# Performance work log

Hardware: AMD Instinct MI355X
Metric: run time of the kernel (lower is better)

The kernel has to match this reference:

```python
import jax, jax.numpy as jnp
import numpy as np

H = 16
D = 64
WIN = 512
THETA = 10000.0


def _rope(x):
    # x: [B, H, T, D]
    T = x.shape[2]
    inv = 1.0 / (THETA ** (jnp.arange(0, D, 2, dtype=jnp.float32) / D))  # [D/2]
    f = jnp.arange(T, dtype=jnp.float32)[:, None] * inv[None, :]          # [T, D/2]
    f = jnp.concatenate([f, f], axis=-1)                                  # [T, D]
    cos, sin = jnp.cos(f), jnp.sin(f)
    x1, x2 = jnp.split(x, 2, axis=-1)
    rot = jnp.concatenate([-x2, x1], axis=-1)
    return x * cos + rot * sin


def setup_inputs() -> dict:
    key = jax.random.key(0)
    ks = jax.random.split(key, 9)
    C = H * D
    s = 0.02
    return {
        "x":  jax.random.normal(ks[0], (2, 2048, C), dtype=jnp.float32),
        "Wq": jax.random.normal(ks[1], (C, C), dtype=jnp.float32) * s,
        "bq": jnp.zeros((C,), dtype=jnp.float32),
        "Wk": jax.random.normal(ks[2], (C, C), dtype=jnp.float32) * s,
        "bk": jnp.zeros((C,), dtype=jnp.float32),
        "Wv": jax.random.normal(ks[3], (C, C), dtype=jnp.float32) * s,
        "bv": jnp.zeros((C,), dtype=jnp.float32),
        "Wo": jax.random.normal(ks[4], (C, C), dtype=jnp.float32) * s,
        "bo": jnp.zeros((C,), dtype=jnp.float32),
    }


def reference(x, Wq, bq, Wk, bk, Wv, bv, Wo, bo):
    B, T, C = x.shape
    def split_heads(y):
        return y.reshape(B, T, H, D).transpose(0, 2, 1, 3)  # [B,H,T,D]
    q = split_heads(x @ Wq + bq)
    k = split_heads(x @ Wk + bk)
    v = split_heads(x @ Wv + bv)
    q = _rope(q)
    k = _rope(k)
    scores = jnp.einsum('bhqd,bhkd->bhqk', q, k) * (1.0 / np.sqrt(D))
    # the original module does NOT apply a causal mask, only the window).
    idx = jnp.arange(T)
    allowed = idx[None, :] >= idx[:, None] - (WIN - 1)      # [T, T] bool
    scores = jnp.where(allowed[None, None], scores, -jnp.inf)
    attn = jax.nn.softmax(scores, axis=-1)
    out = jnp.einsum('bhqk,bhkd->bhqd', attn, v)
    out = out.transpose(0, 2, 1, 3).reshape(B, T, C)
    return out @ Wo + bo
```

## Files before the change

kernel.cpp:

```cpp
#include <hip/hip_runtime.h>
#include <hip/hip_bf16.h>
#include <math.h>

#define Bsz 2
#define Tt  2048
#define Cc  1024
#define Hh  16
#define Dd  64

typedef __attribute__((ext_vector_type(8))) short short8v;
typedef __attribute__((ext_vector_type(4))) short short4v;
typedef __attribute__((ext_vector_type(8))) _Float16 half8v;
typedef __attribute__((ext_vector_type(4))) float f32x4;
typedef __attribute__((ext_vector_type(16))) float f32x16;
typedef __attribute__((ext_vector_type(4))) unsigned int uint4v;

static __device__ __forceinline__ short f2h(float f) {
  _Float16 h = (_Float16)f;
  return __builtin_bit_cast(short, h);
}
static __device__ __forceinline__ float h2f(short s) {
  _Float16 h = __builtin_bit_cast(_Float16, s);
  return (float)h;
}
static __device__ __forceinline__ void gll16(const void* g, void* l) {
  __builtin_amdgcn_global_load_lds((const __attribute__((address_space(1))) unsigned int*)g,
                                   (__attribute__((address_space(3))) unsigned int*)l, 16, 0, 0);
}

__global__ __launch_bounds__(256) void prep(const float* __restrict__ x,
                                            const float* __restrict__ Wq,
                                            const float* __restrict__ Wk,
                                            const float* __restrict__ Wv,
                                            const float* __restrict__ Wo,
                                            short* __restrict__ xh,
                                            short* __restrict__ WTh,
                                            float* __restrict__ rt) {
  __shared__ float T[64][68];
  const int bid = blockIdx.x;
  const int tid = threadIdx.x;

  if (bid < 2048) {
    int t = bid * 256 + tid;
    const float* s = x + (size_t)t * 8;
    float4 a = *(const float4*)s, b = *(const float4*)(s + 4);
    short8v h;
    h[0] = f2h(a.x); h[1] = f2h(a.y); h[2] = f2h(a.z); h[3] = f2h(a.w);
    h[4] = f2h(b.x); h[5] = f2h(b.y); h[6] = f2h(b.z); h[7] = f2h(b.w);
    *(short8v*)(xh + (size_t)t * 8) = h;
  } else if (bid < 3072) {
    const int z = (bid - 2048) >> 8;
    const int slot = (bid - 2048) & 255;
    const float* W = z == 0 ? Wq : z == 1 ? Wk : z == 2 ? Wv : Wo;
    short* oh = WTh + (size_t)z * 1048576;
    const int n0 = (slot & 15) * 64, k0 = (slot >> 4) * 64;
#pragma unroll
    for (int i = 0; i < 4; ++i) {
      int s2 = tid + i * 256;
      int r = s2 >> 4, c4 = (s2 & 15) << 2;
      *(float4*)&T[r][c4] = *(const float4*)(W + (size_t)(k0 + r) * Cc + n0 + c4);
    }
    __syncthreads();
#pragma unroll
    for (int i = 0; i < 2; ++i) {
      int s2 = tid + i * 256;
      int nl = s2 >> 3, ks = (s2 & 7) << 3;
      short8v h;
#pragma unroll
      for (int e = 0; e < 8; ++e) h[e] = f2h(T[ks + e][nl]);
      *(short8v*)(oh + (size_t)(n0 + nl) * Cc + k0 + ks) = h;
    }
  } else {
    int idx = (bid - 3072) * 256 + tid;
    int t = idx >> 5, p = idx & 31;
    float inv = exp2f(-(float)p * (13.2877123795494f / 32.f));
    float sn, cs;
    sincosf((float)t * inv, &sn, &cs);
    float2 v; v.x = cs; v.y = sn;
    *(float2*)(rt + (size_t)idx * 2) = v;
  }
}

__device__ __forceinline__ void core128h(const short* __restrict__ Ah,
                                         const short* __restrict__ Bh,
                                         short* AhL, short* BhL,
                                         int row0, int col0, int wv, int lane, f32x4 acc[4][4]) {
  const int l15 = lane & 15, g = lane >> 4;
  const int wr = wv >> 1, wc = wv & 1;

  const int r8 = lane >> 3;
  const int sch = ((lane & 7) ^ r8) << 3;
  size_t aoff[4], boff[4];
#pragma unroll
  for (int gi = 0; gi < 4; ++gi) {
    aoff[gi] = (size_t)(row0 + wv * 32 + 8 * gi + r8) * Cc + sch;
    boff[gi] = (size_t)(col0 + wv * 32 + 8 * gi + r8) * Cc + sch;
  }
  short* dA = AhL + wv * 2048;
  short* dB = BhL + wv * 2048;

  int aL[4][2], bL[4][2];
#pragma unroll
  for (int m = 0; m < 4; ++m)
#pragma unroll
    for (int s = 0; s < 2; ++s) {
      aL[m][s] = (wr * 64 + m * 16 + l15) * 64 + (((4 * s + g) ^ (l15 & 7)) << 3);
      bL[m][s] = (wc * 64 + m * 16 + l15) * 64 + (((4 * s + g) ^ (l15 & 7)) << 3);
    }

  for (int k0 = 0; k0 < Cc; k0 += 64) {
    __syncthreads();
#pragma unroll
    for (int gi = 0; gi < 4; ++gi) {
      gll16(Ah + aoff[gi] + k0, dA + gi * 512);
      gll16(Bh + boff[gi] + k0, dB + gi * 512);
    }
    __syncthreads();
#pragma unroll
    for (int s = 0; s < 2; ++s) {
      half8v a[4], b[4];
#pragma unroll
      for (int m = 0; m < 4; ++m) a[m] = __builtin_bit_cast(half8v, *(short8v*)&AhL[aL[m][s]]);
#pragma unroll
      for (int n = 0; n < 4; ++n) b[n] = __builtin_bit_cast(half8v, *(short8v*)&BhL[bL[n][s]]);
#pragma unroll
      for (int m = 0; m < 4; ++m)
#pragma unroll
        for (int n = 0; n < 4; ++n)
          acc[m][n] = __builtin_amdgcn_mfma_f32_16x16x32_f16(a[m], b[n], acc[m][n], 0, 0, 0);
    }
  }
}

__global__ __launch_bounds__(256, 3) void gemm_qkv(const short* __restrict__ xh,
                                                   const short* __restrict__ WTh,
                                                   const float* __restrict__ bq,
                                                   const float* __restrict__ bk,
                                                   const float* __restrict__ bv,
                                                   const float* __restrict__ rt,
                                                   short* __restrict__ qb,
                                                   short* __restrict__ kb,
                                                   short* __restrict__ vb) {
  __shared__ short AhL[8192], BhL[8192];
  const int mode = blockIdx.y;
  const short* Bh = WTh + (size_t)mode * 1048576;
  const float* bias = mode == 0 ? bq : mode == 1 ? bk : bv;
  short* Y = mode == 0 ? qb : mode == 1 ? kb : vb;

  const int bid = blockIdx.x;
  const int nid = ((bid & 7) << 5) | (bid >> 3);
  const int row0 = (nid >> 3) * 128, col0 = (nid & 7) * 128;
  const int lane = threadIdx.x & 63, wv = threadIdx.x >> 6;
  const int l15 = lane & 15, g = lane >> 4;
  const int wr = wv >> 1, wc = wv & 1;

  f32x4 acc[4][4];
#pragma unroll
  for (int m = 0; m < 4; ++m)
#pragma unroll
    for (int n = 0; n < 4; ++n) acc[m][n] = (f32x4){0.f, 0.f, 0.f, 0.f};

  core128h(xh, Bh, AhL, BhL, row0, col0, wv, lane, acc);

  const int cbase = col0 + wc * 64;
  const int h = cbase >> 6;
  if (mode < 2) {
    const float scale = (mode == 0) ? 0.18033688f : 1.0f;
    const float2* rt2 = (const float2*)rt;
#pragma unroll
    for (int n = 0; n < 2; ++n) {
      const int d = n * 16 + l15;
      const float b0 = bias[cbase + d], b1 = bias[cbase + d + 32];
#pragma unroll
      for (int m = 0; m < 4; ++m)
#pragma unroll
        for (int rr = 0; rr < 4; ++rr) {
          int R = row0 + wr * 64 + m * 16 + g * 4 + rr;
          int bI = R >> 11, t = R & (Tt - 1);
          float2 cssn = rt2[t * 32 + d];
          float v0 = acc[m][n][rr] + b0, v1 = acc[m][n + 2][rr] + b1;
          size_t base = (((size_t)(bI * Hh + h) * Tt + t) << 6) + d;
          Y[base]      = f2h((v0 * cssn.x - v1 * cssn.y) * scale);
          Y[base + 32] = f2h((v1 * cssn.x + v0 * cssn.y) * scale);
        }
    }
  } else {
#pragma unroll
    for (int n = 0; n < 2; ++n) {
      const int d = n * 16 + l15;
      const float b0 = bias[cbase + d], b1 = bias[cbase + d + 32];
#pragma unroll
      for (int m = 0; m < 4; ++m) {
        int R = row0 + wr * 64 + m * 16 + g * 4;
        int bI = R >> 11, t = R & (Tt - 1);
        short4v s0, s1;
#pragma unroll
        for (int rr = 0; rr < 4; ++rr) {
          s0[rr] = f2h(acc[m][n][rr] + b0);
          s1[rr] = f2h(acc[m][n + 2][rr] + b1);
        }
        size_t base = ((size_t)(bI * Hh + h) * Dd);
        *(short4v*)(Y + (base + d) * Tt + t)      = s0;
        *(short4v*)(Y + (base + d + 32) * Tt + t) = s1;
      }
    }
  }
}

__global__ __launch_bounds__(256, 3) void gemm_out(const short* __restrict__ ah,
                                                   const short* __restrict__ WTo,
                                                   const float* __restrict__ bias,
                                                   float* __restrict__ Y) {
  __shared__ short AhL[8192], BhL[8192];
  const int bid = blockIdx.x;
  const int nid = ((bid & 7) << 5) | (bid >> 3);
  const int row0 = (nid >> 3) * 128, col0 = (nid & 7) * 128;
  const int lane = threadIdx.x & 63, wv = threadIdx.x >> 6;
  const int l15 = lane & 15, g = lane >> 4;
  const int wr = wv >> 1, wc = wv & 1;

  f32x4 acc[4][4];
#pragma unroll
  for (int m = 0; m < 4; ++m)
#pragma unroll
    for (int n = 0; n < 4; ++n) acc[m][n] = (f32x4){0.f, 0.f, 0.f, 0.f};

  core128h(ah, WTo, AhL, BhL, row0, col0, wv, lane, acc);

  const int cbase = col0 + wc * 64;
#pragma unroll
  for (int n = 0; n < 2; ++n) {
    const int ccol = cbase + n * 16 + l15;
    const float b0 = bias[ccol], b1 = bias[ccol + 32];
#pragma unroll
    for (int m = 0; m < 4; ++m)
#pragma unroll
      for (int rr = 0; rr < 4; ++rr) {
        int R = row0 + wr * 64 + m * 16 + g * 4 + rr;
        Y[(size_t)R * Cc + ccol]      = acc[m][n][rr] + b0;
        Y[(size_t)R * Cc + ccol + 32] = acc[m][n + 2][rr] + b1;
      }
  }
}

static __device__ const int JQ2[32] = {0,0, 1,1, 2,2, 3,3, 4,4, 5,5, 6,6, 7,7,
                                       8,8, 9,9, 10,10, 11,11, 12,12, 13,13,
                                       14,14, 15,15};
static __device__ const int JK2[32] = {0,1, 0,1, 0,1, 0,1, 0,1, 0,1, 0,1, 0,1,
                                       0,1, 0,1, 0,1, 0,1, 0,1, 0,1, 0,1, 0,1};

__global__ __launch_bounds__(256, 4) void attn_mfma(const short* __restrict__ q,
                                                    const short* __restrict__ k,
                                                    const short* __restrict__ vT,
                                                    short* __restrict__ ah,
                                                    float* __restrict__ yb,
                                                    float* __restrict__ side) {
  const int n = blockIdx.x;
  const int xcd = n & 7;
  const int t7 = n >> 3;
  const int bhj = t7 & 3;
  const int j = t7 >> 2;
  const int bh = xcd * 4 + bhj;
  const int Q = JQ2[j];
  const int kh = JK2[j];
  const int q0 = Q * 128;

  const int tid = threadIdx.x;
  const int lane = tid & 63;
  const int wv = tid >> 6;
  const int l31 = lane & 31;
  const int hb = lane >> 5;
  const int qbase = q0 + wv * 32;
  const int tq = qbase + l31;

  const short* qgb = q + (size_t)bh * Tt * Dd;
  const short* kgb = k + (size_t)bh * Tt * Dd;
  const short* vgb = vT + (size_t)bh * Dd * Tt;

  const short* qp = qgb + (size_t)tq * Dd + 8 * hb;
  half8v qf[4];
#pragma unroll
  for (int i = 0; i < 4; ++i) qf[i] = __builtin_bit_cast(half8v, *(const short8v*)(qp + 16 * i));

  __shared__ short Klds[2][4096];
  __shared__ short Vt[2][4096];

  const int r8 = lane >> 3;
  const size_t ksrc0 = (size_t)(wv * 16 + r8) * Dd + (((lane & 7) ^ r8) << 3);
  const size_t ksrc1 = ksrc0 + (size_t)8 * Dd;
  const int vlog = ((lane & 7) - r8) & 7;
  const size_t vsrc0 = (size_t)(wv * 16 + r8) * Tt + (vlog << 3);
  const size_t vsrc1 = vsrc0 + (size_t)8 * Tt;

#define STAGE64(BUF, JT)                                                     \
  {                                                                          \
    gll16(kgb + (size_t)(JT) * Dd + ksrc0, &Klds[BUF][wv * 1024]);           \
    gll16(kgb + (size_t)(JT) * Dd + ksrc1, &Klds[BUF][wv * 1024 + 512]);     \
    gll16(vgb + vsrc0 + (JT), &Vt[BUF][wv * 1024]);                          \
    gll16(vgb + vsrc1 + (JT), &Vt[BUF][wv * 1024 + 512]);                    \
  }

  int koff[4], voff[4];
#pragma unroll
  for (int i = 0; i < 4; ++i) {
    koff[i] = l31 * 64 + (((2 * i + hb) ^ (l31 & 7)) << 3);
    voff[i] = l31 * 64 + ((((2 * i + hb) + (l31 & 7)) & 7) << 3);
  }

  f32x16 oacc[2];
#pragma unroll
  for (int t = 0; t < 2; ++t)
#pragma unroll
    for (int r = 0; r < 16; ++r) oacc[t][r] = 0.f;
  float lrun = 0.f;

  const int cs0 = (q0 >= 512) ? (q0 - 511) : 0;
  const int cstart = cs0 & ~63;
  const int nch_b = (Tt - cstart) >> 6;
  const int lower = (nch_b + 1) >> 1;
  const int mystart = cstart + (kh ? (lower << 6) : 0);
  const int myn = kh ? (nch_b - lower) : lower;

  STAGE64(0, mystart);
  __syncthreads();

  int cur = 0;
  for (int ci = 0; ci < myn; ++ci) {
    const int jt = mystart + (ci << 6);

    if (ci + 1 < myn) STAGE64(cur ^ 1, jt + 64);

    const short* kbuf = &Klds[cur][0];
    f32x16 seA, seB;
#pragma unroll
    for (int r = 0; r < 16; ++r) { seA[r] = 0.f; seB[r] = 0.f; }
    __builtin_amdgcn_s_setprio(1);
#pragma unroll
    for (int i = 0; i < 4; ++i) {
      half8v kfA = __builtin_bit_cast(half8v, *(short8v*)&kbuf[koff[i]]);
      seA = __builtin_amdgcn_mfma_f32_32x32x16_f16(kfA, qf[i], seA, 0, 0, 0);
    }
#pragma unroll
    for (int i = 0; i < 4; ++i) {
      half8v kfB = __builtin_bit_cast(half8v, *(short8v*)&kbuf[koff[i] + 2048]);
      seB = __builtin_amdgcn_mfma_f32_32x32x16_f16(kfB, qf[i], seB, 0, 0, 0);
    }
    __builtin_amdgcn_s_setprio(0);

    if (jt < qbase - 480) {
      int th = tq - 511 - jt;
#pragma unroll
      for (int r = 0; r < 16; ++r) {
        int row = (r & 3) + 8 * (r >> 2) + 4 * hb;
        if (row < th) seA[r] = -1e30f;
        if (32 + row < th) seB[r] = -1e30f;
      }
    }

    float pA[16], pB[16];
#pragma unroll
    for (int r = 0; r < 16; ++r) {
      asm("v_exp_f32 %0, %1" : "=v"(pA[r]) : "v"(seA[r]));
      asm("v_exp_f32 %0, %1" : "=v"(pB[r]) : "v"(seB[r]));
    }
    float t0 = 0.f, t1 = 0.f, t2 = 0.f, t3 = 0.f;
#pragma unroll
    for (int r = 0; r < 16; r += 4) {
      t0 += pA[r];     t1 += pA[r + 1]; t2 += pA[r + 2]; t3 += pA[r + 3];
      t0 += pB[r];     t1 += pB[r + 1]; t2 += pB[r + 2]; t3 += pB[r + 3];
    }
    float psum = (t0 + t1) + (t2 + t3);
    psum += __shfl_xor(psum, 32);
    lrun += psum;

    unsigned pa[8], pb[8];
#pragma unroll
    for (int i = 0; i < 8; ++i) {
      pa[i] = __builtin_bit_cast(unsigned, __builtin_amdgcn_cvt_pkrtz(pA[2 * i], pA[2 * i + 1]));
      pb[i] = __builtin_bit_cast(unsigned, __builtin_amdgcn_cvt_pkrtz(pB[2 * i], pB[2 * i + 1]));
    }
    asm volatile("v_permlane32_swap_b32 %0, %1" : "+v"(pa[0]), "+v"(pa[2]));
    asm volatile("v_permlane32_swap_b32 %0, %1" : "+v"(pa[1]), "+v"(pa[3]));
    asm volatile("v_permlane32_swap_b32 %0, %1" : "+v"(pa[4]), "+v"(pa[6]));
    asm volatile("v_permlane32_swap_b32 %0, %1" : "+v"(pa[5]), "+v"(pa[7]));
    asm volatile("v_permlane32_swap_b32 %0, %1" : "+v"(pb[0]), "+v"(pb[2]));
    asm volatile("v_permlane32_swap_b32 %0, %1" : "+v"(pb[1]), "+v"(pb[3]));
    asm volatile("v_permlane32_swap_b32 %0, %1" : "+v"(pb[4]), "+v"(pb[6]));
    asm volatile("v_permlane32_swap_b32 %0, %1" : "+v"(pb[5]), "+v"(pb[7]));
    uint4v fA0, fA1, fB0, fB1;
    fA0[0] = pa[0]; fA0[1] = pa[1]; fA0[2] = pa[2]; fA0[3] = pa[3];
    fA1[0] = pa[4]; fA1[1] = pa[5]; fA1[2] = pa[6]; fA1[3] = pa[7];
    fB0[0] = pb[0]; fB0[1] = pb[1]; fB0[2] = pb[2]; fB0[3] = pb[3];
    fB1[0] = pb[4]; fB1[1] = pb[5]; fB1[2] = pb[6]; fB1[3] = pb[7];
    half8v pfA0 = __builtin_bit_cast(half8v, fA0);
    half8v pfA1 = __builtin_bit_cast(half8v, fA1);
    half8v pfB0 = __builtin_bit_cast(half8v, fB0);
    half8v pfB1 = __builtin_bit_cast(half8v, fB1);

    const short* vbuf = &Vt[cur][0];
    __builtin_amdgcn_s_setprio(1);
#pragma unroll
    for (int t = 0; t < 2; ++t) {
      const int ro = t * 2048;
      half8v v0 = __builtin_bit_cast(half8v, *(short8v*)&vbuf[voff[0] + ro]);
      half8v v1 = __builtin_bit_cast(half8v, *(short8v*)&vbuf[voff[1] + ro]);
      half8v v2 = __builtin_bit_cast(half8v, *(short8v*)&vbuf[voff[2] + ro]);
      half8v v3 = __builtin_bit_cast(half8v, *(short8v*)&vbuf[voff[3] + ro]);
      oacc[t] = __builtin_amdgcn_mfma_f32_32x32x16_f16(v0, pfA0, oacc[t], 0, 0, 0);
      oacc[t] = __builtin_amdgcn_mfma_f32_32x32x16_f16(v1, pfA1, oacc[t], 0, 0, 0);
      oacc[t] = __builtin_amdgcn_mfma_f32_32x32x16_f16(v2, pfB0, oacc[t], 0, 0, 0);
      oacc[t] = __builtin_amdgcn_mfma_f32_32x32x16_f16(v3, pfB1, oacc[t], 0, 0, 0);
    }
    __builtin_amdgcn_s_setprio(0);

    __syncthreads();
    cur ^= 1;
  }

  const float invl = 1.f / lrun;
  const int row = bh * Tt + tq;
  if (hb == 0) side[kh * 65536 + row] = lrun;
  const int bI = bh >> 4, hd = bh & 15;
  if (kh == 0) {
    short* op = ah + ((size_t)(bI * Tt + tq)) * Cc + hd * Dd;
#pragma unroll
    for (int t = 0; t < 2; ++t)
#pragma unroll
      for (int rq = 0; rq < 4; ++rq) {
        short4v hv;
#pragma unroll
        for (int rr = 0; rr < 4; ++rr) hv[rr] = f2h(oacc[t][4 * rq + rr] * invl);
        *(short4v*)(op + 32 * t + 8 * rq + 4 * hb) = hv;
      }
  } else {
    float* yp = yb + (size_t)row * 64;
#pragma unroll
    for (int t = 0; t < 2; ++t)
#pragma unroll
      for (int rq = 0; rq < 4; ++rq) {
        f32x4 o4;
#pragma unroll
        for (int rr = 0; rr < 4; ++rr) o4[rr] = oacc[t][4 * rq + rr] * invl;
        *(f32x4*)(yp + 32 * t + 8 * rq + 4 * hb) = o4;
      }
  }
}

__global__ __launch_bounds__(256) void attn_merge(short* __restrict__ ah,
                                                  const float* __restrict__ yb,
                                                  const float* __restrict__ side) {
  const int bh = blockIdx.y;
  const int idx = blockIdx.x * 256 + threadIdx.x;
  const int tq = idx >> 2;
  const int qd = (idx & 3) << 4;
  const int row = bh * Tt + tq;
  const float l0 = side[row], l1 = side[65536 + row];
  const float inv = 1.f / (l0 + l1);
  const float a0 = l0 * inv, a1 = l1 * inv;

  const int bI = bh >> 4, hd = bh & 15;
  short* op = ah + ((size_t)(bI * Tt + tq)) * Cc + hd * Dd + qd;
  const float* yp = yb + (size_t)row * 64 + qd;

  short8v h0 = *(short8v*)op, h1 = *(short8v*)(op + 8);
  short8v o0, o1;
#pragma unroll
  for (int e = 0; e < 8; ++e) o0[e] = f2h(a0 * h2f(h0[e]) + a1 * yp[e]);
#pragma unroll
  for (int e = 0; e < 8; ++e) o1[e] = f2h(a0 * h2f(h1[e]) + a1 * yp[8 + e]);
  *(short8v*)op = o0;
  *(short8v*)(op + 8) = o1;
}

extern "C" void kernel_launch(void* const* d_in, const int* in_sizes, int n_in,
                              void* d_out, int out_size, void* d_ws, size_t ws_size,
                              hipStream_t stream) {
  const float* x  = (const float*)d_in[0];
  const float* Wq = (const float*)d_in[1];
  const float* bq = (const float*)d_in[2];
  const float* Wk = (const float*)d_in[3];
  const float* bk = (const float*)d_in[4];
  const float* Wv = (const float*)d_in[5];
  const float* bv = (const float*)d_in[6];
  const float* Wo = (const float*)d_in[7];
  const float* bo = (const float*)d_in[8];

  short* ws16 = (short*)d_ws;
  short* xh  = ws16;
  short* WTh = ws16 + 4194304;
  short* qb  = ws16 + 8388608;
  short* kb  = ws16 + 12582912;
  short* vb  = ws16 + 16777216;
  short* ah  = ws16 + 20971520;
  float* yb   = (float*)(ws16 + 25165824);
  float* side = yb + 4194304;
  float* rt   = side + 131072;

  prep<<<3328, 256, 0, stream>>>(x, Wq, Wk, Wv, Wo, xh, WTh, rt);

  gemm_qkv<<<dim3(256, 3), 256, 0, stream>>>(xh, WTh, bq, bk, bv, rt, qb, kb, vb);

  attn_mfma<<<1024, 256, 0, stream>>>(qb, kb, vb, ah, yb, side);
  attn_merge<<<dim3(32, 32), 256, 0, stream>>>(ah, yb, side);

  gemm_out<<<256, 256, 0, stream>>>(ah, WTh + 3 * 1048576, bo, (float*)d_out);
}
```

Before: 114.3 us.

## Split attention KV range three ways, store fp16 partials, retile output GEMM to 128x64

Attention work is split across three key-range chunks per query block instead of two, raising the grid from 1024 to 1536 blocks. Partial outputs for the non-first chunks are stored as fp16 rather than fp32, and the merge kernel combines three partials weighted by their softmax denominators. The output GEMM gets its own inline 128x64 tile loop with 512 blocks and higher occupancy in place of the shared 128x128 core. This aims to fill the GPU better and cut partial-buffer traffic, at the cost of more merge reads, lower precision in the partials and smaller GEMM tiles with less data reuse.

```diff
diff --git a/kernel.cpp b/kernel.cpp
--- a/kernel.cpp
+++ b/kernel.cpp
@@ -207,53 +207,97 @@
   }
 }
 
-__global__ __launch_bounds__(256, 3) void gemm_out(const short* __restrict__ ah,
+__global__ __launch_bounds__(256, 4) void gemm_out(const short* __restrict__ ah,
                                                    const short* __restrict__ WTo,
                                                    const float* __restrict__ bias,
                                                    float* __restrict__ Y) {
-  __shared__ short AhL[8192], BhL[8192];
+  __shared__ short AhL[8192], BhL[4096];
   const int bid = blockIdx.x;
-  const int nid = ((bid & 7) << 5) | (bid >> 3);
-  const int row0 = (nid >> 3) * 128, col0 = (nid & 7) * 128;
+  const int nid = ((bid & 7) << 6) | (bid >> 3);
+  const int row0 = (nid >> 4) * 128, col0 = (nid & 15) * 64;
   const int lane = threadIdx.x & 63, wv = threadIdx.x >> 6;
   const int l15 = lane & 15, g = lane >> 4;
-  const int wr = wv >> 1, wc = wv & 1;
-
-  f32x4 acc[4][4];
-#pragma unroll
-  for (int m = 0; m < 4; ++m)
+
+  const int r8 = lane >> 3;
+  const int sch = ((lane & 7) ^ r8) << 3;
+  size_t aoff[4], boff[2];
+#pragma unroll
+  for (int gi = 0; gi < 4; ++gi)
+    aoff[gi] = (size_t)(row0 + wv * 32 + 8 * gi + r8) * Cc + sch;
+#pragma unroll
+  for (int gi = 0; gi < 2; ++gi)
+    boff[gi] = (size_t)(col0 + wv * 16 + 8 * gi + r8) * Cc + sch;
+  short* dA = AhL + wv * 2048;
+  short* dB = BhL + wv * 1024;
+
+  int aL[2][2], bL[4][2];
+#pragma unroll
+  for (int m = 0; m < 2; ++m)
+#pragma unroll
+    for (int s = 0; s < 2; ++s)
+      aL[m][s] = (wv * 32 + m * 16 + l15) * 64 + (((4 * s + g) ^ (l15 & 7)) << 3);
+#pragma unroll
+  for (int n = 0; n < 4; ++n)
+#pragma unroll
+    for (int s = 0; s < 2; ++s)
+      bL[n][s] = (n * 16 + l15) * 64 + (((4 * s + g) ^ (l15 & 7)) << 3);
+
+  f32x4 acc[2][4];
+#pragma unroll
+  for (int m = 0; m < 2; ++m)
 #pragma unroll
     for (int n = 0; n < 4; ++n) acc[m][n] = (f32x4){0.f, 0.f, 0.f, 0.f};
 
-  core128h(ah, WTo, AhL, BhL, row0, col0, wv, lane, acc);
-
-  const int cbase = col0 + wc * 64;
-#pragma unroll
-  for (int n = 0; n < 2; ++n) {
-    const int ccol = cbase + n * 16 + l15;
-    const float b0 = bias[ccol], b1 = bias[ccol + 32];
-#pragma unroll
-    for (int m = 0; m < 4; ++m)
+  for (int k0 = 0; k0 < Cc; k0 += 64) {
+    __syncthreads();
+#pragma unroll
+    for (int gi = 0; gi < 4; ++gi) gll16(ah + aoff[gi] + k0, dA + gi * 512);
+#pragma unroll
+    for (int gi = 0; gi < 2; ++gi) gll16(WTo + boff[gi] + k0, dB + gi * 512);
+    __syncthreads();
+#pragma unroll
+    for (int s = 0; s < 2; ++s) {
+      half8v a[2], b[4];
+#pragma unroll
+      for (int m = 0; m < 2; ++m) a[m] = __builtin_bit_cast(half8v, *(short8v*)&AhL[aL[m][s]]);
+#pragma unroll
+      for (int n = 0; n < 4; ++n) b[n] = __builtin_bit_cast(half8v, *(short8v*)&BhL[bL[n][s]]);
+#pragma unroll
+      for (int m = 0; m < 2; ++m)
+#pragma unroll
+        for (int n = 0; n < 4; ++n)
+          acc[m][n] = __builtin_amdgcn_mfma_f32_16x16x32_f16(a[m], b[n], acc[m][n], 0, 0, 0);
+    }
+  }
+
+#pragma unroll
+  for (int n = 0; n < 4; ++n) {
+    const int ccol = col0 + n * 16 + l15;
+    const float b0 = bias[ccol];
+#pragma unroll
+    for (int m = 0; m < 2; ++m)
 #pragma unroll
       for (int rr = 0; rr < 4; ++rr) {
-        int R = row0 + wr * 64 + m * 16 + g * 4 + rr;
-        Y[(size_t)R * Cc + ccol]      = acc[m][n][rr] + b0;
-        Y[(size_t)R * Cc + ccol + 32] = acc[m][n + 2][rr] + b1;
+        int R = row0 + wv * 32 + m * 16 + g * 4 + rr;
+        Y[(size_t)R * Cc + ccol] = acc[m][n][rr] + b0;
       }
   }
 }
 
-static __device__ const int JQ2[32] = {0,0, 1,1, 2,2, 3,3, 4,4, 5,5, 6,6, 7,7,
-                                       8,8, 9,9, 10,10, 11,11, 12,12, 13,13,
-                                       14,14, 15,15};
-static __device__ const int JK2[32] = {0,1, 0,1, 0,1, 0,1, 0,1, 0,1, 0,1, 0,1,
-                                       0,1, 0,1, 0,1, 0,1, 0,1, 0,1, 0,1, 0,1};
+static __device__ const int JQ3[48] = {0,0,0, 1,1,1, 2,2,2, 3,3,3, 4,4,4, 5,5,5,
+                                       6,6,6, 7,7,7, 8,8,8, 9,9,9, 10,10,10,
+                                       11,11,11, 12,12,12, 13,13,13, 14,14,14,
+                                       15,15,15};
+static __device__ const int JK3[48] = {0,1,2, 0,1,2, 0,1,2, 0,1,2, 0,1,2, 0,1,2,
+                                       0,1,2, 0,1,2, 0,1,2, 0,1,2, 0,1,2, 0,1,2,
+                                       0,1,2, 0,1,2, 0,1,2, 0,1,2};
 
 __global__ __launch_bounds__(256, 4) void attn_mfma(const short* __restrict__ q,
                                                     const short* __restrict__ k,
                                                     const short* __restrict__ vT,
                                                     short* __restrict__ ah,
-                                                    float* __restrict__ yb,
+                                                    short* __restrict__ p1,
+                                                    short* __restrict__ p2,
                                                     float* __restrict__ side) {
   const int n = blockIdx.x;
   const int xcd = n & 7;
@@ -261,8 +305,8 @@
   const int bhj = t7 & 3;
   const int j = t7 >> 2;
   const int bh = xcd * 4 + bhj;
-  const int Q = JQ2[j];
-  const int kh = JK2[j];
+  const int Q = JQ3[j];
+  const int kh = JK3[j];
   const int q0 = Q * 128;
 
   const int tid = threadIdx.x;
@@ -317,9 +361,10 @@
   const int cs0 = (q0 >= 512) ? (q0 - 511) : 0;
   const int cstart = cs0 & ~63;
   const int nch_b = (Tt - cstart) >> 6;
-  const int lower = (nch_b + 1) >> 1;
-  const int mystart = cstart + (kh ? (lower << 6) : 0);
-  const int myn = kh ? (nch_b - lower) : lower;
+  const int start_i = (nch_b * kh) / 3;
+  const int end_i = (nch_b * (kh + 1)) / 3;
+  const int mystart = cstart + (start_i << 6);
+  const int myn = end_i - start_i;
 
   STAGE64(0, mystart);
   __syncthreads();
@@ -433,41 +478,47 @@
         *(short4v*)(op + 32 * t + 8 * rq + 4 * hb) = hv;
       }
   } else {
-    float* yp = yb + (size_t)row * 64;
+    short* pp = (kh == 1 ? p1 : p2) + (size_t)row * 64;
 #pragma unroll
     for (int t = 0; t < 2; ++t)
 #pragma unroll
       for (int rq = 0; rq < 4; ++rq) {
-        f32x4 o4;
-#pragma unroll
-        for (int rr = 0; rr < 4; ++rr) o4[rr] = oacc[t][4 * rq + rr] * invl;
-        *(f32x4*)(yp + 32 * t + 8 * rq + 4 * hb) = o4;
+        short4v hv;
+#pragma unroll
+        for (int rr = 0; rr < 4; ++rr) hv[rr] = f2h(oacc[t][4 * rq + rr] * invl);
+        *(short4v*)(pp + 32 * t + 8 * rq + 4 * hb) = hv;
       }
   }
 }
 
 __global__ __launch_bounds__(256) void attn_merge(short* __restrict__ ah,
-                                                  const float* __restrict__ yb,
+                                                  const short* __restrict__ p1,
+                                                  const short* __restrict__ p2,
                                                   const float* __restrict__ side) {
   const int bh = blockIdx.y;
   const int idx = blockIdx.x * 256 + threadIdx.x;
   const int tq = idx >> 2;
   const int qd = (idx & 3) << 4;
   const int row = bh * Tt + tq;
-  const float l0 = side[row], l1 = side[65536 + row];
-  const float inv = 1.f / (l0 + l1);
-  const float a0 = l0 * inv, a1 = l1 * inv;
+  const float l0 = side[row], l1 = side[65536 + row], l2 = side[131072 + row];
+  const float inv = 1.f / (l0 + l1 + l2);
+  const float a0 = l0 * inv, a1 = l1 * inv, a2 = l2 * inv;
 
   const int bI = bh >> 4, hd = bh & 15;
   short* op = ah + ((size_t)(bI * Tt + tq)) * Cc + hd * Dd + qd;
-  const float* yp = yb + (size_t)row * 64 + qd;
-
-  short8v h0 = *(short8v*)op, h1 = *(short8v*)(op + 8);
+  const short* r1 = p1 + (size_t)row * 64 + qd;
+  const short* r2 = p2 + (size_t)row * 64 + qd;
+
+  short8v h0 = *(short8v*)op,        h1 = *(short8v*)(op + 8);
+  short8v u0 = *(const short8v*)r1,  u1 = *(const short8v*)(r1 + 8);
+  short8v w0 = *(const short8v*)r2,  w1 = *(const short8v*)(r2 + 8);
   short8v o0, o1;
 #pragma unroll
-  for (int e = 0; e < 8; ++e) o0[e] = f2h(a0 * h2f(h0[e]) + a1 * yp[e]);
-#pragma unroll
-  for (int e = 0; e < 8; ++e) o1[e] = f2h(a0 * h2f(h1[e]) + a1 * yp[8 + e]);
+  for (int e = 0; e < 8; ++e)
+    o0[e] = f2h(a0 * h2f(h0[e]) + a1 * h2f(u0[e]) + a2 * h2f(w0[e]));
+#pragma unroll
+  for (int e = 0; e < 8; ++e)
+    o1[e] = f2h(a0 * h2f(h1[e]) + a1 * h2f(u1[e]) + a2 * h2f(w1[e]));
   *(short8v*)op = o0;
   *(short8v*)(op + 8) = o1;
 }
@@ -492,16 +543,17 @@
   short* kb  = ws16 + 12582912;
   short* vb  = ws16 + 16777216;
   short* ah  = ws16 + 20971520;
-  float* yb   = (float*)(ws16 + 25165824);
-  float* side = yb + 4194304;
-  float* rt   = side + 131072;
+  short* p1  = ws16 + 25165824;
+  short* p2  = ws16 + 29360128;
+  float* side = (float*)(ws16 + 33554432);
+  float* rt   = side + 196608;
 
   prep<<<3328, 256, 0, stream>>>(x, Wq, Wk, Wv, Wo, xh, WTh, rt);
 
   gemm_qkv<<<dim3(256, 3), 256, 0, stream>>>(xh, WTh, bq, bk, bv, rt, qb, kb, vb);
 
-  attn_mfma<<<1024, 256, 0, stream>>>(qb, kb, vb, ah, yb, side);
-  attn_merge<<<dim3(32, 32), 256, 0, stream>>>(ah, yb, side);
-
-  gemm_out<<<256, 256, 0, stream>>>(ah, WTh + 3 * 1048576, bo, (float*)d_out);
-}
+  attn_mfma<<<1536, 256, 0, stream>>>(qb, kb, vb, ah, p1, p2, side);
+  attn_merge<<<dim3(32, 32), 256, 0, stream>>>(ah, p1, p2, side);
+
+  gemm_out<<<512, 256, 0, stream>>>(ah, WTh + 3 * 1048576, bo, (float*)d_out);
+}
```

Result: faster. 111.8 us (-2.2%).
